# Kernel optimization log

Hardware: AMD Instinct MI355X
Metric: run time of the kernel (lower is better)

The kernel has to match this reference:

```python
import jax, jax.numpy as jnp
import numpy as np

N_POINTS = 262144
NUM_LEVELS = 16
LEVEL_DIM = 8
BASE_RES = 16
LOG2_HASH = 21
BOUNDS = 10.0
TEXT_REP = 512
IMAGE_REP = 512
MLP_WIDTH = 256
PRIMES = (1, 2654435761, 805459861)  # instant-NGP fast_hash primes


def _level_layout():
    # mirrors torch-ngp GridEncoder offset computation
    max_params = 2 ** LOG2_HASH
    sizes, offsets = [], [0]
    for l in range(NUM_LEVELS):
        res = int(np.ceil(BASE_RES * (2.0 ** l)))
        p = min(max_params, res ** 3)
        p = int(np.ceil(p / 8) * 8)  # align to 8
        sizes.append(p)
        offsets.append(offsets[-1] + p)
    return sizes, offsets

SIZES, OFFSETS = _level_layout()
TOTAL_PARAMS = OFFSETS[-1]  # ~27.56M rows


def grid_encode(u, embeddings):
    """u: [N,3] in [0,1]; torch-ngp kernel remaps with bound=1: u=(u+1)/2.
    With this config (res+1)^3 > hashmap_size at every level, so the hash
    path is always taken (faithful to get_grid_index)."""
    u = (u + 1.0) * 0.5
    feats = []
    for l in range(NUM_LEVELS):
        scale = 2.0 ** l * BASE_RES - 1.0          # exp2(l*log2(s))*H - 1
        pos = u * scale + 0.5                       # align_corners=False
        base = jnp.floor(pos)
        frac = pos - base                           # [N,3] trilinear fracs
        pg = base.astype(jnp.uint32)
        acc = jnp.zeros((u.shape[0], LEVEL_DIM), dtype=u.dtype)
        for corner in range(8):
            bits = [(corner >> d) & 1 for d in range(3)]
            cpos = pg + jnp.asarray(bits, dtype=jnp.uint32)
            w = jnp.prod(jnp.where(jnp.asarray(bits, dtype=bool), frac, 1.0 - frac), axis=-1)
            h = (cpos[:, 0] * jnp.uint32(PRIMES[0])
                 ^ cpos[:, 1] * jnp.uint32(PRIMES[1])
                 ^ cpos[:, 2] * jnp.uint32(PRIMES[2]))  # uint32 wraparound hash
            idx = (h % jnp.uint32(SIZES[l])).astype(jnp.int32) + OFFSETS[l]
            acc = acc + w[:, None] * embeddings[idx]    # gather [N,8]
        feats.append(acc)
    return jnp.concatenate(feats, axis=-1)              # [N, 128]


def setup_inputs() -> dict:
    key = jax.random.key(0)
    ks = jax.random.split(key, 8)
    x = jax.random.uniform(ks[0], (N_POINTS, 3), jnp.float32, -BOUNDS, BOUNDS)
    emb = jax.random.uniform(ks[1], (TOTAL_PARAMS, LEVEL_DIM), jnp.float32, -1e-4, 1e-4)
    d_in = NUM_LEVELS * LEVEL_DIM  # 128
    d_out = TEXT_REP + IMAGE_REP   # 1024
    W1 = jax.random.normal(ks[2], (d_in, MLP_WIDTH), jnp.float32) * (1.0 / np.sqrt(d_in))
    b1 = jnp.zeros((MLP_WIDTH,), jnp.float32)
    W2 = jax.random.normal(ks[3], (MLP_WIDTH, MLP_WIDTH), jnp.float32) * (1.0 / np.sqrt(MLP_WIDTH))
    b2 = jnp.zeros((MLP_WIDTH,), jnp.float32)
    W3 = jax.random.normal(ks[4], (MLP_WIDTH, d_out), jnp.float32) * (1.0 / np.sqrt(MLP_WIDTH))
    b3 = jnp.zeros((d_out,), jnp.float32)
    return {"x": x, "embeddings": emb, "W1": W1, "b1": b1, "W2": W2, "b2": b2, "W3": W3, "b3": b3}


def reference(x, embeddings, W1, b1, W2, b2, W3, b3):
    # bound normalization: (x - min) / (max - min), min=-10, max=+10
    bounded = (x + BOUNDS) / (2.0 * BOUNDS)
    gh = grid_encode(bounded, embeddings)
    h = jax.nn.relu(gh @ W1 + b1)
    h = jax.nn.relu(h @ W2 + b2)
    out = h @ W3 + b3
    label_latent = out[..., :TEXT_REP]
    image_latent = out[..., TEXT_REP:TEXT_REP + IMAGE_REP]  # image head = Identity
    return (label_latent, image_latent)
```

## Files before the change

kernel.cpp:

```cpp
#include <hip/hip_runtime.h>
#include <cstdint>

#pragma STDC FP_CONTRACT OFF


typedef _Float16 f16;
typedef __attribute__((ext_vector_type(8))) _Float16 f16x8;
typedef __attribute__((ext_vector_type(4))) float f32x4;

#define ACT_SCALE 4096.0f
#define INV_ACT_SCALE (1.0f / 4096.0f)

__device__ __forceinline__ void gld16(const void* g, void* l) {
  __builtin_amdgcn_global_load_lds(
      (const __attribute__((address_space(1))) void*)(uintptr_t)g,
      (__attribute__((address_space(3))) void*)(uint32_t)(uintptr_t)l,
      16, 0, 0);
}

__global__ __launch_bounds__(256) void grid_encode_kernel(
    const float* __restrict__ x, const float* __restrict__ emb,
    f16* __restrict__ gh, int p0, int npts)
{
#pragma clang fp contract(off)
  int g = blockIdx.x * blockDim.x + threadIdx.x;
  if (g >= npts * 16) return;
  int pl = g >> 4;
  int l  = g & 15;
  int p  = p0 + pl;

  float x0 = x[3 * p + 0];
  float x1 = x[3 * p + 1];
  float x2 = x[3 * p + 2];

  float t0 = (x0 + 10.0f) * 0.05f;
  float t1 = (x1 + 10.0f) * 0.05f;
  float t2 = (x2 + 10.0f) * 0.05f;
  asm volatile("" : "+v"(t0), "+v"(t1), "+v"(t2));
  float u0 = (t0 + 1.0f) * 0.5f;
  float u1 = (t1 + 1.0f) * 0.5f;
  float u2 = (t2 + 1.0f) * 0.5f;
  asm volatile("" : "+v"(u0), "+v"(u1), "+v"(u2));

  float scale = (float)((16 << l) - 1);
  float pos0 = u0 * scale + 0.5f;
  float pos1 = u1 * scale + 0.5f;
  float pos2 = u2 * scale + 0.5f;

  float fb0 = floorf(pos0), fb1 = floorf(pos1), fb2 = floorf(pos2);
  float f0 = pos0 - fb0;
  float f1 = pos1 - fb1;
  float f2 = pos2 - fb2;
  uint32_t px = (uint32_t)fb0, py = (uint32_t)fb1, pz = (uint32_t)fb2;

  uint32_t mask = (l < 3) ? ((4096u << (3 * l)) - 1u) : 2097151u;
  uint32_t off;
  if (l == 0)      off = 0u;
  else if (l == 1) off = 4096u;
  else if (l == 2) off = 36864u;
  else             off = 299008u + (uint32_t)(l - 3) * 2097152u;

  float wx[2] = {1.0f - f0, f0};
  float wy[2] = {1.0f - f1, f1};
  float wz[2] = {1.0f - f2, f2};

  float acc[8];
#pragma unroll
  for (int j = 0; j < 8; ++j) acc[j] = 0.0f;

#pragma unroll
  for (int c = 0; c < 8; ++c) {
    uint32_t cx = px + (uint32_t)(c & 1);
    uint32_t cy = py + (uint32_t)((c >> 1) & 1);
    uint32_t cz = pz + (uint32_t)((c >> 2) & 1);
    float w = wx[c & 1] * wy[(c >> 1) & 1] * wz[(c >> 2) & 1];
    uint32_t h = cx ^ (cy * 2654435761u) ^ (cz * 805459861u);
    uint32_t idx = (h & mask) + off;
    const float4* e = (const float4*)(emb + (size_t)idx * 8);
    float4 e0 = e[0];
    float4 e1 = e[1];
    float m0 = w * e0.x, m1 = w * e0.y, m2 = w * e0.z, m3 = w * e0.w;
    float m4 = w * e1.x, m5 = w * e1.y, m6 = w * e1.z, m7 = w * e1.w;
    asm volatile("" : "+v"(m0), "+v"(m1), "+v"(m2), "+v"(m3),
                      "+v"(m4), "+v"(m5), "+v"(m6), "+v"(m7));
    acc[0] += m0; acc[1] += m1; acc[2] += m2; acc[3] += m3;
    acc[4] += m4; acc[5] += m5; acc[6] += m6; acc[7] += m7;
  }

  f16x8 o;
#pragma unroll
  for (int j = 0; j < 8; ++j) o[j] = (f16)(acc[j] * ACT_SCALE);
  *(f16x8*)&gh[(size_t)pl * 128 + l * 8] = o;
}

template <int K, int N>
__global__ __launch_bounds__(256) void prep_w(
    const float* __restrict__ W, f16* __restrict__ Wt)
{
  int i = blockIdx.x * 256 + threadIdx.x;
  if (i >= N * K) return;
  int n = i / K, k = i - n * K;
  Wt[i] = (f16)W[(size_t)k * N + n];
}

__global__ __launch_bounds__(256) void prep_w1f(
    const float* __restrict__ W1, f16* __restrict__ Wf1)
{
  int i = blockIdx.x * 256 + threadIdx.x;
  if (i >= 128 * 256) return;
  int e  = i & 7;
  int lr = (i >> 3) & 15;
  int kg = (i >> 7) & 15;
  int q  = i >> 11;
  int n = q * 16 + lr;
  int k = kg * 8 + e;
  Wf1[i] = (f16)W1[(size_t)k * 256 + n];
}

__global__ __launch_bounds__(256) void prep_w2f(
    const float* __restrict__ W2, f16* __restrict__ Wf2)
{
  int i = blockIdx.x * 256 + threadIdx.x;
  if (i >= 256 * 256) return;
  int e  = i & 7;
  int lr = (i >> 3) & 15;
  int kg = (i >> 7) & 31;
  int q  = i >> 12;
  int n = q * 16 + lr;
  int k = kg * 8 + e;
  Wf2[i] = (f16)W2[(size_t)k * 256 + n];
}

__global__ __launch_bounds__(512) void fused_mlp(
    const f16* __restrict__ gh, const f16* __restrict__ Wf1,
    const float* __restrict__ b1, const f16* __restrict__ Wf2,
    const float* __restrict__ b2, const f16* __restrict__ Wt3,
    const float* __restrict__ b3, float* __restrict__ out,
    int rowBase, int nTotal)
{
  __shared__ alignas(16) f16 As2[3][4096];
  __shared__ alignas(16) f16 H1[128 * 256];
  __shared__ alignas(16) f16 H2[128 * 256];
  __shared__ float B3s[1024];

  const int tid  = threadIdx.x;
  const int lane = tid & 63;
  const int wid  = tid >> 6;
  const int bm   = blockIdx.x * 128;
  const int lr   = lane & 15;
  const int lkg  = lane >> 4;

  auto stage3 = [&](int buf, int c) {
    const int g   = tid;
    const int row = g >> 5;
    const int sg  = g & 31;
    const int gs  = (sg & 24) | ((sg ^ row) & 7);
    gld16(&Wt3[(size_t)(c * 16 + row) * 256 + gs * 8], &As2[buf][g * 8]);
  };

#pragma unroll
  for (int s = 0; s < 4; ++s) {
    const int g   = tid + s * 512;
    const int row = g >> 4;
    const int sg  = g & 15;
    const int gs  = (sg & 8) | ((sg ^ row) & 7);
    gld16(&gh[(size_t)(bm + row) * 128 + gs * 8], &H2[g * 8]);
  }
  stage3(0, 0);
  stage3(1, 1);
  stage3(2, 2);
  B3s[tid] = b3[tid];
  B3s[tid + 512] = b3[tid + 512];
  __syncthreads();

  {
    const int rowg = wid >> 2, colg = wid & 3;
    f16x8 bf1[4][4];
#pragma unroll
    for (int j = 0; j < 4; ++j)
#pragma unroll
      for (int f = 0; f < 4; ++f)
        bf1[j][f] = *(const f16x8*)&Wf1[(((colg * 4 + j) * 16 + f * 4 + lkg) * 16 + lr) * 8];

    f32x4 acc[4][4];
#pragma unroll
    for (int i = 0; i < 4; ++i)
#pragma unroll
      for (int j = 0; j < 4; ++j) acc[i][j] = (f32x4){0.f, 0.f, 0.f, 0.f};

#pragma unroll
    for (int f = 0; f < 4; ++f) {
      f16x8 af[4];
#pragma unroll
      for (int i = 0; i < 4; ++i) {
        const int r  = rowg * 64 + i * 16 + lr;
        const int kg = f * 4 + lkg;
        const int gs = (kg & 8) | ((kg ^ r) & 7);
        af[i] = *(const f16x8*)&H2[r * 128 + gs * 8];
      }
#pragma unroll
      for (int i = 0; i < 4; ++i)
#pragma unroll
        for (int j = 0; j < 4; ++j)
          acc[i][j] = __builtin_amdgcn_mfma_f32_16x16x32_f16(
              af[i], bf1[j][f], acc[i][j], 0, 0, 0);
    }

#pragma unroll
    for (int i = 0; i < 4; ++i)
#pragma unroll
      for (int j = 0; j < 4; ++j) {
        const int col = colg * 64 + j * 16 + lr;
        const float bv = b1[col];
        const int kg = col >> 3, e = col & 7;
#pragma unroll
        for (int q = 0; q < 4; ++q) {
          const int row = rowg * 64 + i * 16 + lkg * 4 + q;
          const int kgs = (kg & 24) | ((kg ^ row) & 7);
          float v = fmaxf(acc[i][j][q] + bv * ACT_SCALE, 0.0f);
          H1[row * 256 + kgs * 8 + e] = (f16)v;
        }
      }
  }
  __syncthreads();

  {
    const int rowg = wid >> 2, colg = wid & 3;
    f16x8 bf2[4][8];
#pragma unroll
    for (int j = 0; j < 4; ++j)
#pragma unroll
      for (int f = 0; f < 8; ++f)
        bf2[j][f] = *(const f16x8*)&Wf2[(((colg * 4 + j) * 32 + f * 4 + lkg) * 16 + lr) * 8];

    f32x4 acc[4][4];
#pragma unroll
    for (int i = 0; i < 4; ++i)
#pragma unroll
      for (int j = 0; j < 4; ++j) acc[i][j] = (f32x4){0.f, 0.f, 0.f, 0.f};

#pragma unroll
    for (int f = 0; f < 8; ++f) {
      f16x8 af[4];
#pragma unroll
      for (int i = 0; i < 4; ++i) {
        const int r   = rowg * 64 + i * 16 + lr;
        const int kg  = f * 4 + lkg;
        const int kgs = (kg & 24) | ((kg ^ r) & 7);
        af[i] = *(const f16x8*)&H1[r * 256 + kgs * 8];
      }
#pragma unroll
      for (int i = 0; i < 4; ++i)
#pragma unroll
        for (int j = 0; j < 4; ++j)
          acc[i][j] = __builtin_amdgcn_mfma_f32_16x16x32_f16(
              af[i], bf2[j][f], acc[i][j], 0, 0, 0);
    }

#pragma unroll
    for (int i = 0; i < 4; ++i)
#pragma unroll
      for (int j = 0; j < 4; ++j) {
        const int col = colg * 64 + j * 16 + lr;
        const float bv = b2[col];
        const int kg = col >> 3, e = col & 7;
#pragma unroll
        for (int q = 0; q < 4; ++q) {
          const int row = rowg * 64 + i * 16 + lkg * 4 + q;
          const int kgs = (kg & 24) | ((kg ^ row) & 7);
          float v = fmaxf(acc[i][j][q] + bv * ACT_SCALE, 0.0f);
          H2[row * 256 + kgs * 8 + e] = (f16)v;
        }
      }
  }
  __syncthreads();

  f16x8 af3[8];
#pragma unroll
  for (int f = 0; f < 8; ++f) {
    const int r   = wid * 16 + lr;
    const int kg  = f * 4 + lkg;
    const int kgs = (kg & 24) | ((kg ^ r) & 7);
    af3[f] = *(const f16x8*)&H2[r * 256 + kgs * 8];
  }

  auto body3 = [&](int c, int wmode, bool dostage) {
    if (wmode == 9) {
      asm volatile("s_waitcnt vmcnt(9)" ::: "memory");
      __builtin_amdgcn_sched_barrier(0);
    } else if (wmode == 8) {
      asm volatile("s_waitcnt vmcnt(8)" ::: "memory");
      __builtin_amdgcn_sched_barrier(0);
    }
    const int buf = c % 3;
    f16x8 bf3[8];
#pragma unroll
    for (int f = 0; f < 8; ++f) {
      const int kg  = f * 4 + lkg;
      const int kgs = (kg & 24) | ((kg ^ lr) & 7);
      bf3[f] = *(const f16x8*)&As2[buf][(lr * 32 + kgs) * 8];
    }
    const int col = c * 16 + lr;
    const float bv = B3s[col];
    asm volatile("s_waitcnt lgkmcnt(0)" ::: "memory");
    __builtin_amdgcn_sched_barrier(0);
    __builtin_amdgcn_s_barrier();
    __builtin_amdgcn_sched_barrier(0);
    if (dostage) stage3(buf, c + 3);
    f32x4 a = (f32x4){0.f, 0.f, 0.f, 0.f};
#pragma unroll
    for (int f = 0; f < 8; ++f)
      a = __builtin_amdgcn_mfma_f32_16x16x32_f16(af3[f], bf3[f], a, 0, 0, 0);
#pragma unroll
    for (int q = 0; q < 4; ++q) {
      const int row = bm + wid * 16 + lkg * 4 + q;
      float v = a[q] * INV_ACT_SCALE + bv;
      size_t grow = (size_t)(rowBase + row);
      float* dst = (col < 512)
                       ? (out + grow * 512 + col)
                       : (out + (size_t)nTotal * 512 + grow * 512 + (col - 512));
      *dst = v;
    }
  };

  body3(0, 0, true);
  body3(1, 0, true);
  for (int c = 2; c <= 60; ++c) body3(c, 9, true);
  body3(61, 9, false);
  body3(62, 8, false);
  body3(63, 0, false);
}

extern "C" void kernel_launch(void* const* d_in, const int* in_sizes, int n_in,
                              void* d_out, int out_size, void* d_ws, size_t ws_size,
                              hipStream_t stream)
{
  const float* x   = (const float*)d_in[0];
  const float* emb = (const float*)d_in[1];
  const float* W1  = (const float*)d_in[2];
  const float* b1  = (const float*)d_in[3];
  const float* W2  = (const float*)d_in[4];
  const float* b2  = (const float*)d_in[5];
  const float* W3  = (const float*)d_in[6];
  const float* b3  = (const float*)d_in[7];
  float* out = (float*)d_out;

  const int NPTS = in_sizes[0] / 3;

  f16* Wf1 = (f16*)d_ws;
  f16* Wf2 = Wf1 + 128 * 256;
  f16* Wt3 = Wf2 + 256 * 256;
  f16* gh0 = Wt3 + 256 * 1024;
  const size_t wtBytes = (size_t)(128 * 256 + 256 * 256 + 256 * 1024) * sizeof(f16);

  long long cmax = (long long)((ws_size - wtBytes) / 256);
  int C = (int)((cmax / 128) * 128);
  if (C > NPTS) C = NPTS;
  if (C < 128) C = 128;

  prep_w1f<<<(128 * 256 + 255) / 256, 256, 0, stream>>>(W1, Wf1);
  prep_w2f<<<(256 * 256 + 255) / 256, 256, 0, stream>>>(W2, Wf2);
  prep_w<256, 1024><<<(256 * 1024 + 255) / 256, 256, 0, stream>>>(W3, Wt3);

  for (int p0 = 0; p0 < NPTS; p0 += C) {
    int cur = (NPTS - p0 < C) ? (NPTS - p0) : C;

    int nthr = cur * 16;
    grid_encode_kernel<<<(nthr + 255) / 256, 256, 0, stream>>>(x, emb, gh0, p0, cur);

    fused_mlp<<<cur / 128, 512, 0, stream>>>(gh0, Wf1, b1, Wf2, b2, Wt3, b3,
                                             out, p0, NPTS);
  }
}
```

Measured before the change: 833.6 us.

## Widen layer-3 column chunks to 32 and stage W3 tiles into freed H1

The final GEMM now processes 32 output columns per step instead of 16, so each of 32 steps issues two MFMA chains from one staged tile. This halves the number of LDS barriers and loop iterations. The separate As2 buffer is removed and W3 tiles are triple-buffered in the H1 scratch area, which is free after layer 2. To allow that, the initial W3 prefetch is moved after layer 2 and loses its overlap with layers 1–2. The vmcnt thresholds are raised to match the larger per-step load and store counts. Output stores are now nontemporal to reduce cache pollution from the large streaming output.

```diff
diff --git a/kernel.cpp b/kernel.cpp
--- a/kernel.cpp
+++ b/kernel.cpp
@@ -138,7 +138,6 @@
     const float* __restrict__ b3, float* __restrict__ out,
     int rowBase, int nTotal)
 {
-  __shared__ alignas(16) f16 As2[3][4096];
   __shared__ alignas(16) f16 H1[128 * 256];
   __shared__ alignas(16) f16 H2[128 * 256];
   __shared__ float B3s[1024];
@@ -151,11 +150,15 @@
   const int lkg  = lane >> 4;
 
   auto stage3 = [&](int buf, int c) {
-    const int g   = tid;
-    const int row = g >> 5;
-    const int sg  = g & 31;
-    const int gs  = (sg & 24) | ((sg ^ row) & 7);
-    gld16(&Wt3[(size_t)(c * 16 + row) * 256 + gs * 8], &As2[buf][g * 8]);
+#pragma unroll
+    for (int s = 0; s < 2; ++s) {
+      const int g   = tid + s * 512;
+      const int row = g >> 5;
+      const int sg  = g & 31;
+      const int gs  = (sg & 24) | ((sg ^ row) & 7);
+      gld16(&Wt3[(size_t)(c * 32 + row) * 256 + gs * 8],
+            &H1[buf * 8192 + g * 8]);
+    }
   };
 
 #pragma unroll
@@ -166,9 +169,6 @@
     const int gs  = (sg & 8) | ((sg ^ row) & 7);
     gld16(&gh[(size_t)(bm + row) * 128 + gs * 8], &H2[g * 8]);
   }
-  stage3(0, 0);
-  stage3(1, 1);
-  stage3(2, 2);
   B3s[tid] = b3[tid];
   B3s[tid + 512] = b3[tid + 512];
   __syncthreads();
@@ -284,51 +284,67 @@
     af3[f] = *(const f16x8*)&H2[r * 256 + kgs * 8];
   }
 
+  stage3(0, 0);
+  stage3(1, 1);
+  stage3(2, 2);
+  __syncthreads();
+
   auto body3 = [&](int c, int wmode, bool dostage) {
-    if (wmode == 9) {
-      asm volatile("s_waitcnt vmcnt(9)" ::: "memory");
+    if (wmode == 18) {
+      asm volatile("s_waitcnt vmcnt(18)" ::: "memory");
       __builtin_amdgcn_sched_barrier(0);
-    } else if (wmode == 8) {
-      asm volatile("s_waitcnt vmcnt(8)" ::: "memory");
+    } else if (wmode == 16) {
+      asm volatile("s_waitcnt vmcnt(16)" ::: "memory");
       __builtin_amdgcn_sched_barrier(0);
     }
     const int buf = c % 3;
-    f16x8 bf3[8];
-#pragma unroll
-    for (int f = 0; f < 8; ++f) {
-      const int kg  = f * 4 + lkg;
-      const int kgs = (kg & 24) | ((kg ^ lr) & 7);
-      bf3[f] = *(const f16x8*)&As2[buf][(lr * 32 + kgs) * 8];
-    }
-    const int col = c * 16 + lr;
-    const float bv = B3s[col];
+    f16x8 bf3[2][8];
+#pragma unroll
+    for (int cg = 0; cg < 2; ++cg)
+#pragma unroll
+      for (int f = 0; f < 8; ++f) {
+        const int n   = cg * 16 + lr;
+        const int kg  = f * 4 + lkg;
+        const int kgs = (kg & 24) | ((kg ^ n) & 7);
+        bf3[cg][f] = *(const f16x8*)&H1[buf * 8192 + (n * 32 + kgs) * 8];
+      }
     asm volatile("s_waitcnt lgkmcnt(0)" ::: "memory");
     __builtin_amdgcn_sched_barrier(0);
     __builtin_amdgcn_s_barrier();
     __builtin_amdgcn_sched_barrier(0);
     if (dostage) stage3(buf, c + 3);
-    f32x4 a = (f32x4){0.f, 0.f, 0.f, 0.f};
-#pragma unroll
-    for (int f = 0; f < 8; ++f)
-      a = __builtin_amdgcn_mfma_f32_16x16x32_f16(af3[f], bf3[f], a, 0, 0, 0);
-#pragma unroll
-    for (int q = 0; q < 4; ++q) {
-      const int row = bm + wid * 16 + lkg * 4 + q;
-      float v = a[q] * INV_ACT_SCALE + bv;
-      size_t grow = (size_t)(rowBase + row);
-      float* dst = (col < 512)
-                       ? (out + grow * 512 + col)
-                       : (out + (size_t)nTotal * 512 + grow * 512 + (col - 512));
-      *dst = v;
+    f32x4 a[2];
+#pragma unroll
+    for (int cg = 0; cg < 2; ++cg) {
+      a[cg] = (f32x4){0.f, 0.f, 0.f, 0.f};
+#pragma unroll
+      for (int f = 0; f < 8; ++f)
+        a[cg] = __builtin_amdgcn_mfma_f32_16x16x32_f16(af3[f], bf3[cg][f],
+                                                       a[cg], 0, 0, 0);
+    }
+#pragma unroll
+    for (int cg = 0; cg < 2; ++cg) {
+      const int col = c * 32 + cg * 16 + lr;
+      const float bv = B3s[col];
+#pragma unroll
+      for (int q = 0; q < 4; ++q) {
+        const int row = bm + wid * 16 + lkg * 4 + q;
+        float v = a[cg][q] * INV_ACT_SCALE + bv;
+        size_t grow = (size_t)(rowBase + row);
+        float* dst = (col < 512)
+                         ? (out + grow * 512 + col)
+                         : (out + (size_t)nTotal * 512 + grow * 512 + (col - 512));
+        __builtin_nontemporal_store(v, dst);
+      }
     }
   };
 
-  body3(0, 0, true);
-  body3(1, 0, true);
-  for (int c = 2; c <= 60; ++c) body3(c, 9, true);
-  body3(61, 9, false);
-  body3(62, 8, false);
-  body3(63, 0, false);
+  body3(0, 18, true);
+  body3(1, 18, true);
+  for (int c = 2; c <= 28; ++c) body3(c, 18, true);
+  body3(29, 18, false);
+  body3(30, 16, false);
+  body3(31, 16, false);
 }
 
 extern "C" void kernel_launch(void* const* d_in, const int* in_sizes, int n_in,
```

After: 767.6 us. -7.9%, faster.

## Halve MLP row tile and reuse activation LDS as W3 ring buffer

Applied to the files above, without the earlier changes.

The fused MLP block now processes 64 rows instead of 128. The separate W3 staging buffers are gone: W3 tiles of 32 columns are streamed into a three-slot ring carved out of the H1/H2 activation buffers once those are no longer needed. Together these cut shared memory per block substantially, and the layer-2 weight fragments are loaded in two halves to lower register pressure, so more blocks can be resident per CU under the new launch bound. Output stores become nontemporal. The cost is more per-block overhead, since each block still loads the W1/W2 fragments and the bias for half as many rows, and the vmcnt wait counts must match the new load/store mix exactly.

```diff
diff --git a/kernel.cpp b/kernel.cpp
--- a/kernel.cpp
+++ b/kernel.cpp
@@ -131,50 +131,56 @@
   Wf2[i] = (f16)W2[(size_t)k * 256 + n];
 }
 
-__global__ __launch_bounds__(512) void fused_mlp(
+__global__ __launch_bounds__(512, 4) void fused_mlp(
     const f16* __restrict__ gh, const f16* __restrict__ Wf1,
     const float* __restrict__ b1, const f16* __restrict__ Wf2,
     const float* __restrict__ b2, const f16* __restrict__ Wt3,
     const float* __restrict__ b3, float* __restrict__ out,
     int rowBase, int nTotal)
 {
-  __shared__ alignas(16) f16 As2[3][4096];
-  __shared__ alignas(16) f16 H1[128 * 256];
-  __shared__ alignas(16) f16 H2[128 * 256];
+  __shared__ alignas(16) f16 H1[64 * 256];
+  __shared__ alignas(16) f16 H2[64 * 256];
   __shared__ float B3s[1024];
 
   const int tid  = threadIdx.x;
   const int lane = tid & 63;
   const int wid  = tid >> 6;
-  const int bm   = blockIdx.x * 128;
+  const int bm   = blockIdx.x * 64;
   const int lr   = lane & 15;
   const int lkg  = lane >> 4;
 
-  auto stage3 = [&](int buf, int c) {
-    const int g   = tid;
-    const int row = g >> 5;
-    const int sg  = g & 31;
-    const int gs  = (sg & 24) | ((sg ^ row) & 7);
-    gld16(&Wt3[(size_t)(c * 16 + row) * 256 + gs * 8], &As2[buf][g * 8]);
+  auto ringbuf = [&](int b) -> f16* {
+    return (b == 0) ? &H1[0] : (b == 1) ? &H1[8192] : &H2[0];
   };
 
-#pragma unroll
-  for (int s = 0; s < 4; ++s) {
+  auto stage3 = [&](int c) {
+    f16* dst = ringbuf(c % 3);
+#pragma unroll
+    for (int s = 0; s < 2; ++s) {
+      const int g   = tid + s * 512;
+      const int row = g >> 5;
+      const int sg  = g & 31;
+      const int gs  = (sg & 24) | ((sg ^ row) & 7);
+      gld16(&Wt3[(size_t)(c * 32 + row) * 256 + gs * 8], &dst[g * 8]);
+    }
+  };
+
+#pragma unroll
+  for (int s = 0; s < 2; ++s) {
     const int g   = tid + s * 512;
     const int row = g >> 4;
     const int sg  = g & 15;
     const int gs  = (sg & 8) | ((sg ^ row) & 7);
     gld16(&gh[(size_t)(bm + row) * 128 + gs * 8], &H2[g * 8]);
   }
-  stage3(0, 0);
-  stage3(1, 1);
-  stage3(2, 2);
   B3s[tid] = b3[tid];
   B3s[tid + 512] = b3[tid + 512];
   __syncthreads();
 
+  const int rowg = wid >> 2;
+  const int colg = wid & 3;
+
   {
-    const int rowg = wid >> 2, colg = wid & 3;
     f16x8 bf1[4][4];
 #pragma unroll
     for (int j = 0; j < 4; ++j)
@@ -182,24 +188,24 @@
       for (int f = 0; f < 4; ++f)
         bf1[j][f] = *(const f16x8*)&Wf1[(((colg * 4 + j) * 16 + f * 4 + lkg) * 16 + lr) * 8];
 
-    f32x4 acc[4][4];
-#pragma unroll
-    for (int i = 0; i < 4; ++i)
+    f32x4 acc[2][4];
+#pragma unroll
+    for (int i = 0; i < 2; ++i)
 #pragma unroll
       for (int j = 0; j < 4; ++j) acc[i][j] = (f32x4){0.f, 0.f, 0.f, 0.f};
 
 #pragma unroll
     for (int f = 0; f < 4; ++f) {
-      f16x8 af[4];
-#pragma unroll
-      for (int i = 0; i < 4; ++i) {
-        const int r  = rowg * 64 + i * 16 + lr;
+      f16x8 af[2];
+#pragma unroll
+      for (int i = 0; i < 2; ++i) {
+        const int r  = rowg * 32 + i * 16 + lr;
         const int kg = f * 4 + lkg;
         const int gs = (kg & 8) | ((kg ^ r) & 7);
         af[i] = *(const f16x8*)&H2[r * 128 + gs * 8];
       }
 #pragma unroll
-      for (int i = 0; i < 4; ++i)
+      for (int i = 0; i < 2; ++i)
 #pragma unroll
         for (int j = 0; j < 4; ++j)
           acc[i][j] = __builtin_amdgcn_mfma_f32_16x16x32_f16(
@@ -207,7 +213,7 @@
     }
 
 #pragma unroll
-    for (int i = 0; i < 4; ++i)
+    for (int i = 0; i < 2; ++i)
 #pragma unroll
       for (int j = 0; j < 4; ++j) {
         const int col = colg * 64 + j * 16 + lr;
@@ -215,7 +221,7 @@
         const int kg = col >> 3, e = col & 7;
 #pragma unroll
         for (int q = 0; q < 4; ++q) {
-          const int row = rowg * 64 + i * 16 + lkg * 4 + q;
+          const int row = rowg * 32 + i * 16 + lkg * 4 + q;
           const int kgs = (kg & 24) | ((kg ^ row) & 7);
           float v = fmaxf(acc[i][j][q] + bv * ACT_SCALE, 0.0f);
           H1[row * 256 + kgs * 8 + e] = (f16)v;
@@ -225,40 +231,43 @@
   __syncthreads();
 
   {
-    const int rowg = wid >> 2, colg = wid & 3;
-    f16x8 bf2[4][8];
-#pragma unroll
-    for (int j = 0; j < 4; ++j)
-#pragma unroll
-      for (int f = 0; f < 8; ++f)
-        bf2[j][f] = *(const f16x8*)&Wf2[(((colg * 4 + j) * 32 + f * 4 + lkg) * 16 + lr) * 8];
-
-    f32x4 acc[4][4];
-#pragma unroll
-    for (int i = 0; i < 4; ++i)
+    f32x4 acc[2][4];
+#pragma unroll
+    for (int i = 0; i < 2; ++i)
 #pragma unroll
       for (int j = 0; j < 4; ++j) acc[i][j] = (f32x4){0.f, 0.f, 0.f, 0.f};
 
 #pragma unroll
-    for (int f = 0; f < 8; ++f) {
-      f16x8 af[4];
-#pragma unroll
-      for (int i = 0; i < 4; ++i) {
-        const int r   = rowg * 64 + i * 16 + lr;
-        const int kg  = f * 4 + lkg;
-        const int kgs = (kg & 24) | ((kg ^ r) & 7);
-        af[i] = *(const f16x8*)&H1[r * 256 + kgs * 8];
+    for (int h = 0; h < 2; ++h) {
+      f16x8 bf2[4][4];
+#pragma unroll
+      for (int j = 0; j < 4; ++j)
+#pragma unroll
+        for (int f = 0; f < 4; ++f)
+          bf2[j][f] = *(const f16x8*)
+              &Wf2[(((colg * 4 + j) * 32 + (h * 4 + f) * 4 + lkg) * 16 + lr) * 8];
+
+#pragma unroll
+      for (int f = 0; f < 4; ++f) {
+        f16x8 af[2];
+#pragma unroll
+        for (int i = 0; i < 2; ++i) {
+          const int r   = rowg * 32 + i * 16 + lr;
+          const int kg  = (h * 4 + f) * 4 + lkg;
+          const int kgs = (kg & 24) | ((kg ^ r) & 7);
+          af[i] = *(const f16x8*)&H1[r * 256 + kgs * 8];
+        }
+#pragma unroll
+        for (int i = 0; i < 2; ++i)
+#pragma unroll
+          for (int j = 0; j < 4; ++j)
+            acc[i][j] = __builtin_amdgcn_mfma_f32_16x16x32_f16(
+                af[i], bf2[j][f], acc[i][j], 0, 0, 0);
       }
-#pragma unroll
-      for (int i = 0; i < 4; ++i)
-#pragma unroll
-        for (int j = 0; j < 4; ++j)
-          acc[i][j] = __builtin_amdgcn_mfma_f32_16x16x32_f16(
-              af[i], bf2[j][f], acc[i][j], 0, 0, 0);
-    }
-
-#pragma unroll
-    for (int i = 0; i < 4; ++i)
+    }
+
+#pragma unroll
+    for (int i = 0; i < 2; ++i)
 #pragma unroll
       for (int j = 0; j < 4; ++j) {
         const int col = colg * 64 + j * 16 + lr;
@@ -266,7 +275,7 @@
         const int kg = col >> 3, e = col & 7;
 #pragma unroll
         for (int q = 0; q < 4; ++q) {
-          const int row = rowg * 64 + i * 16 + lkg * 4 + q;
+          const int row = rowg * 32 + i * 16 + lkg * 4 + q;
           const int kgs = (kg & 24) | ((kg ^ row) & 7);
           float v = fmaxf(acc[i][j][q] + bv * ACT_SCALE, 0.0f);
           H2[row * 256 + kgs * 8 + e] = (f16)v;
@@ -275,60 +284,71 @@
   }
   __syncthreads();
 
+  const int wr = wid & 3;
+  const int wc = wid >> 2;
+
   f16x8 af3[8];
 #pragma unroll
   for (int f = 0; f < 8; ++f) {
-    const int r   = wid * 16 + lr;
+    const int r   = wr * 16 + lr;
     const int kg  = f * 4 + lkg;
     const int kgs = (kg & 24) | ((kg ^ r) & 7);
     af3[f] = *(const f16x8*)&H2[r * 256 + kgs * 8];
   }
+  stage3(0);
+  stage3(1);
+  __syncthreads();
+  stage3(2);
 
   auto body3 = [&](int c, int wmode, bool dostage) {
-    if (wmode == 9) {
-      asm volatile("s_waitcnt vmcnt(9)" ::: "memory");
+    if (wmode == 10) {
+      asm volatile("s_waitcnt vmcnt(10)" ::: "memory");
       __builtin_amdgcn_sched_barrier(0);
     } else if (wmode == 8) {
       asm volatile("s_waitcnt vmcnt(8)" ::: "memory");
       __builtin_amdgcn_sched_barrier(0);
-    }
-    const int buf = c % 3;
+    } else if (wmode == 6) {
+      asm volatile("s_waitcnt vmcnt(6)" ::: "memory");
+      __builtin_amdgcn_sched_barrier(0);
+    }
+    const f16* buf = ringbuf(c % 3);
     f16x8 bf3[8];
 #pragma unroll
     for (int f = 0; f < 8; ++f) {
+      const int n   = wc * 16 + lr;
       const int kg  = f * 4 + lkg;
-      const int kgs = (kg & 24) | ((kg ^ lr) & 7);
-      bf3[f] = *(const f16x8*)&As2[buf][(lr * 32 + kgs) * 8];
-    }
-    const int col = c * 16 + lr;
-    const float bv = B3s[col];
+      const int kgs = (kg & 24) | ((kg ^ n) & 7);
+      bf3[f] = *(const f16x8*)&buf[(n * 32 + kgs) * 8];
+    }
     asm volatile("s_waitcnt lgkmcnt(0)" ::: "memory");
     __builtin_amdgcn_sched_barrier(0);
     __builtin_amdgcn_s_barrier();
     __builtin_amdgcn_sched_barrier(0);
-    if (dostage) stage3(buf, c + 3);
+    if (dostage) stage3(c + 3);
     f32x4 a = (f32x4){0.f, 0.f, 0.f, 0.f};
 #pragma unroll
     for (int f = 0; f < 8; ++f)
       a = __builtin_amdgcn_mfma_f32_16x16x32_f16(af3[f], bf3[f], a, 0, 0, 0);
+    const int col = c * 32 + wc * 16 + lr;
+    const float bv = B3s[col];
 #pragma unroll
     for (int q = 0; q < 4; ++q) {
-      const int row = bm + wid * 16 + lkg * 4 + q;
+      const int row = bm + wr * 16 + lkg * 4 + q;
       float v = a[q] * INV_ACT_SCALE + bv;
       size_t grow = (size_t)(rowBase + row);
       float* dst = (col < 512)
                        ? (out + grow * 512 + col)
                        : (out + (size_t)nTotal * 512 + grow * 512 + (col - 512));
-      *dst = v;
+      __builtin_nontemporal_store(v, dst);
     }
   };
 
   body3(0, 0, true);
-  body3(1, 0, true);
-  for (int c = 2; c <= 60; ++c) body3(c, 9, true);
-  body3(61, 9, false);
-  body3(62, 8, false);
-  body3(63, 0, false);
+  body3(1, 6, true);
+  for (int c = 2; c <= 28; ++c) body3(c, 10, true);
+  body3(29, 10, false);
+  body3(30, 8, false);
+  body3(31, 8, false);
 }
 
 extern "C" void kernel_launch(void* const* d_in, const int* in_sizes, int n_in,
@@ -368,7 +388,7 @@
     int nthr = cur * 16;
     grid_encode_kernel<<<(nthr + 255) / 256, 256, 0, stream>>>(x, emb, gh0, p0, cur);
 
-    fused_mlp<<<cur / 128, 512, 0, stream>>>(gh0, Wf1, b1, Wf2, b2, Wt3, b3,
-                                             out, p0, NPTS);
-  }
-}
+    fused_mlp<<<cur / 64, 512, 0, stream>>>(gh0, Wf1, b1, Wf2, b2, Wt3, b3,
+                                            out, p0, NPTS);
+  }
+}
```

Result: faster. 788.9 us (-5.4%).
